# Performance work log

Hardware: AMD Instinct MI355X
Metric: run time of the kernel (lower is better)

## Reference

```python
import jax, jax.numpy as jnp
import numpy as np
import math

B, N, C = 4, 2048, 768
H = 12
DFF = 4 * C
EPS = 1e-5

def _layernorm(x, gamma, beta):
    mu = jnp.mean(x, axis=-1, keepdims=True)
    var = jnp.var(x, axis=-1, keepdims=True)
    return (x - mu) * jax.lax.rsqrt(var + EPS) * gamma + beta

def setup_inputs() -> dict:
    key = jax.random.key(0)
    ks = jax.random.split(key, 12)
    s = 0.02
    return {
        "x": jax.random.normal(ks[0], (B, N, C), jnp.float32),
        "Wqkv": jax.random.normal(ks[1], (C, 3 * C), jnp.float32) * s,
        "bqkv": jnp.zeros((3 * C,), jnp.float32),
        "Wproj": jax.random.normal(ks[2], (C, C), jnp.float32) * s,
        "bproj": jnp.zeros((C,), jnp.float32),
        "g1": jnp.ones((C,), jnp.float32),
        "b1": jnp.zeros((C,), jnp.float32),
        "g2": jnp.ones((C,), jnp.float32),
        "b2": jnp.zeros((C,), jnp.float32),
        "Wfc1": jax.random.normal(ks[3], (C, DFF), jnp.float32) * s,
        "bfc1": jnp.zeros((DFF,), jnp.float32),
        "Wfc2": jax.random.normal(ks[4], (DFF, C), jnp.float32) * s,
        "bfc2": jnp.zeros((C,), jnp.float32),
    }

def reference(x, Wqkv, bqkv, Wproj, bproj, g1, b1, g2, b2, Wfc1, bfc1, Wfc2, bfc2):
    head_dim = C // H
    qkv = x @ Wqkv + bqkv                      # [B,N,3C]
    q, k, v = jnp.split(qkv, 3, axis=-1)
    # [B,N,C] -> [B,H,N,hd]
    def to_heads(t):
        return t.reshape(B, N, H, head_dim).transpose(0, 2, 1, 3)
    q, k, v = to_heads(q), to_heads(k), to_heads(v)
    attn = jnp.einsum('bhqd,bhkd->bhqk', q, k) / math.sqrt(head_dim)
    attn = jax.nn.softmax(attn, axis=-1)       # dropout p=0 -> identity
    out = jnp.einsum('bhqk,bhkd->bhqd', attn, v)
    out = out.transpose(0, 2, 1, 3).reshape(B, N, C)
    out = out @ Wproj + bproj
    x = _layernorm(x + out, g1, b1)
    h = jax.nn.gelu(x @ Wfc1 + bfc1, approximate=False) @ Wfc2 + bfc2
    x = _layernorm(x + h, g2, b2)
    return x
```

## Files before the change

kernel.cpp:

```cpp
#include <hip/hip_runtime.h>

typedef __bf16 bf16;
typedef __bf16 bf16x2 __attribute__((ext_vector_type(2)));
typedef __bf16 bf16x4 __attribute__((ext_vector_type(4)));
typedef __bf16 bf16x8 __attribute__((ext_vector_type(8)));
typedef float  f32x4  __attribute__((ext_vector_type(4)));
typedef float  f32x16 __attribute__((ext_vector_type(16)));
typedef int    intx4  __attribute__((ext_vector_type(4)));

#define BB 4
#define SEQ 2048
#define CH 768
#define NH 12
#define HD 64
#define DFF 3072
#define MROWS (BB * SEQ)
#define C3 (3 * CH)

__device__ inline f32x16 mfma32(bf16x8 a, bf16x8 b, f32x16 c) {
    return __builtin_amdgcn_mfma_f32_32x32x16_bf16(a, b, c, 0, 0, 0);
}
__device__ inline f32x4 mfma16(bf16x8 a, bf16x8 b, f32x4 c) {
    return __builtin_amdgcn_mfma_f32_16x16x32_bf16(a, b, c, 0, 0, 0);
}
__device__ inline void gload16(const void* g, void* l) {
    __builtin_amdgcn_global_load_lds((const __attribute__((address_space(1))) void*)g,
                                     (__attribute__((address_space(3))) void*)l, 16, 0, 0);
}

__global__ void cvt_f32_bf16(const float* __restrict__ in, bf16* __restrict__ out, int n) {
    int i = (blockIdx.x * blockDim.x + threadIdx.x) * 4;
    if (i + 3 >= n) {
        for (int j = 0; j < 4 && i + j < n; ++j) out[i + j] = (bf16)in[i + j];
        return;
    }
    f32x4 v = *(const f32x4*)&in[i];
    bf16x4 o;
    #pragma unroll
    for (int j = 0; j < 4; ++j) o[j] = (bf16)v[j];
    *(bf16x4*)&out[i] = o;
}

__global__ void transpose_cvt(const float* __restrict__ in, bf16* __restrict__ out, int R, int Cc) {
    __shared__ bf16 t[32][33];
    int tx = threadIdx.x & 31, ty = threadIdx.x >> 5;
    int c0 = blockIdx.x * 32, r0 = blockIdx.y * 32;
    #pragma unroll
    for (int i = 0; i < 32; i += 8)
        t[ty + i][tx] = (bf16)in[(size_t)(r0 + ty + i) * Cc + c0 + tx];
    __syncthreads();
    #pragma unroll
    for (int i = 0; i < 32; i += 8)
        out[(size_t)(c0 + ty + i) * R + r0 + tx] = t[tx][ty + i];
}

__global__ void transpose_v(const bf16* __restrict__ qkvb, bf16* __restrict__ vt) {
    __shared__ bf16 t[32][33];
    int tx = threadIdx.x & 31, ty = threadIdx.x >> 5;
    int n0 = blockIdx.x * 32, d0 = blockIdx.y * 32, bh = blockIdx.z;
    int b = bh / NH, h = bh - b * NH;
    #pragma unroll
    for (int i = 0; i < 32; i += 8)
        t[ty + i][tx] = qkvb[((size_t)b * SEQ + n0 + ty + i) * C3 + 2 * CH + h * HD + d0 + tx];
    __syncthreads();
    #pragma unroll
    for (int i = 0; i < 32; i += 8)
        vt[((size_t)bh * HD + d0 + ty + i) * SEQ + n0 + tx] = t[tx][ty + i];
}

template <int OMODE>
__global__ __launch_bounds__(256) void gemm_bt(const bf16* __restrict__ A,
                                               const bf16* __restrict__ Bt,
                                               const float* __restrict__ bias,
                                               void* __restrict__ Cout,
                                               int M, int N, int K) {
    __shared__ __align__(16) bf16 As[128][32];
    __shared__ __align__(16) bf16 Bs[128][32];
    const int bm = blockIdx.y * 128, bn = blockIdx.x * 128;
    const int tid = threadIdx.x;
    const int lane = tid & 63, w = tid >> 6;
    const int wr = w >> 1, wc = w & 1;
    const int lr = lane & 15, lg = lane >> 4;

    const int srow = tid >> 2, schk = (tid & 3) * 8;
    const bf16* gA0 = A + (size_t)(bm + srow) * K + schk;
    const bf16* gA1 = A + (size_t)(bm + 64 + srow) * K + schk;
    const bf16* gB0 = Bt + (size_t)(bn + srow) * K + schk;
    const bf16* gB1 = Bt + (size_t)(bn + 64 + srow) * K + schk;
    bf16* lA0 = &As[srow][schk];
    bf16* lA1 = &As[64 + srow][schk];
    bf16* lB0 = &Bs[srow][schk];
    bf16* lB1 = &Bs[64 + srow][schk];

    f32x4 acc[4][4];
    #pragma unroll
    for (int i = 0; i < 4; ++i)
        #pragma unroll
        for (int j = 0; j < 4; ++j) acc[i][j] = (f32x4){0.f, 0.f, 0.f, 0.f};

    for (int k0 = 0; k0 < K; k0 += 32) {
        __syncthreads();
        gload16(gA0, lA0); gload16(gA1, lA1);
        gload16(gB0, lB0); gload16(gB1, lB1);
        gA0 += 32; gA1 += 32; gB0 += 32; gB1 += 32;
        __syncthreads();
        bf16x8 af[4], bfr[4];
        #pragma unroll
        for (int mi = 0; mi < 4; ++mi)
            af[mi] = *(const bf16x8*)&As[wr * 64 + mi * 16 + lr][lg * 8];
        #pragma unroll
        for (int ni = 0; ni < 4; ++ni)
            bfr[ni] = *(const bf16x8*)&Bs[wc * 64 + ni * 16 + lr][lg * 8];
        #pragma unroll
        for (int mi = 0; mi < 4; ++mi)
            #pragma unroll
            for (int ni = 0; ni < 4; ++ni)
                acc[mi][ni] = mfma16(af[mi], bfr[ni], acc[mi][ni]);
    }

    #pragma unroll
    for (int mi = 0; mi < 4; ++mi) {
        #pragma unroll
        for (int ni = 0; ni < 4; ++ni) {
            int col = bn + wc * 64 + ni * 16 + lr;
            float bsv = bias[col];
            #pragma unroll
            for (int r = 0; r < 4; ++r) {
                int row = bm + wr * 64 + mi * 16 + lg * 4 + r;
                float v = acc[mi][ni][r] + bsv;
                if (OMODE == 2) v = 0.5f * v * (1.0f + erff(v * 0.70710678118654752f));
                if (OMODE == 0)
                    ((float*)Cout)[(size_t)row * N + col] = v;
                else
                    ((bf16*)Cout)[(size_t)row * N + col] = (bf16)v;
            }
        }
    }
}

#define C2F 0.18033688011112f
#define THR2 11.5416f
__global__ __launch_bounds__(256, 3) void attn_kernel(const bf16* __restrict__ qkvb,
                                                      const bf16* __restrict__ vt,
                                                      bf16* __restrict__ outb) {
    __shared__ __align__(16) bf16 Kl[2][64 * 64];
    __shared__ __align__(16) bf16 Vl[2][64 * 64];
    const int tid = threadIdx.x;
    const int w = tid >> 6, lane = tid & 63;
    const int lq = lane & 31;
    const int hi = lane >> 5;
    const int lin = blockIdx.x;
    const int xcd = lin & 7, slot = lin >> 3;
    const int bh = xcd * 6 + (slot >> 4);
    const int qt = slot & 15;
    const int b = bh / NH, h = bh - b * NH;
    const int q0 = qt * 128 + w * 32;

    const bf16* qbase = qkvb + (size_t)b * SEQ * C3 + h * HD;
    const bf16* kbase = qbase + CH;
    const bf16* vbase = vt + (size_t)bh * HD * SEQ;

    const int srow = tid >> 3;
    const int ksc = (tid & 7) ^ (srow & 7);
    const bf16* gk0 = kbase + (size_t)srow * C3 + ksc * 8;
    const bf16* gk1 = kbase + (size_t)(srow + 32) * C3 + ksc * 8;
    const bf16* gv0 = vbase + (size_t)srow * SEQ + ksc * 8;
    const bf16* gv1 = vbase + (size_t)(srow + 32) * SEQ + ksc * 8;
    const int ldst = tid * 8;

    bf16x8 qf[4];
    #pragma unroll
    for (int ks = 0; ks < 4; ++ks)
        qf[ks] = *(const bf16x8*)&qbase[(size_t)(q0 + lq) * C3 + ks * 16 + hi * 8];

    f32x16 o0 = {0.f}, o1 = {0.f};
    float m = -3.0e38f, l = 0.f;

    const int swz = lq & 7;

    auto stage = [&](int buf, int kv0) {
        gload16(gk0 + (size_t)kv0 * C3, &Kl[buf][ldst]);
        gload16(gk1 + (size_t)kv0 * C3, &Kl[buf][2048 + ldst]);
        gload16(gv0 + kv0, &Vl[buf][ldst]);
        gload16(gv1 + kv0, &Vl[buf][2048 + ldst]);
    };

    auto process = [&](const bf16* Kb, const bf16* Vb) {
        f32x16 st0 = {0.f}, st1 = {0.f};
        #pragma unroll
        for (int ks = 0; ks < 4; ++ks) {
            int c = 8 * ((2 * ks + hi) ^ swz);
            bf16x8 k0 = *(const bf16x8*)&Kb[lq * 64 + c];
            bf16x8 k1 = *(const bf16x8*)&Kb[(32 + lq) * 64 + c];
            st0 = mfma32(k0, qf[ks], st0);
            st1 = mfma32(k1, qf[ks], st1);
        }
        float t_[8];
        #pragma unroll
        for (int r = 0; r < 8; ++r)
            t_[r] = fmaxf(fmaxf(st0[r], st0[r + 8]), fmaxf(st1[r], st1[r + 8]));
        #pragma unroll
        for (int r = 0; r < 4; ++r) t_[r] = fmaxf(t_[r], t_[r + 4]);
        float mx = fmaxf(fmaxf(t_[0], t_[1]), fmaxf(t_[2], t_[3]));
        mx = fmaxf(mx, __shfl_xor(mx, 32));
        float m2x = mx * C2F;
        if (!__all(m2x <= m + THR2)) {
            float mn = fmaxf(m, m2x);
            float alpha = __builtin_amdgcn_exp2f(m - mn);
            m = mn;
            l *= alpha;
            #pragma unroll
            for (int r = 0; r < 16; ++r) {
                int qr = (r & 3) + 8 * (r >> 2) + 4 * hi;
                float ar = __shfl(alpha, qr);
                o0[r] *= ar;
                o1[r] *= ar;
            }
        }
        bf16x8 pa[4];
        float ps0, ps1;
        {
            float p[16];
            #pragma unroll
            for (int r = 0; r < 16; ++r) p[r] = __builtin_amdgcn_exp2f(fmaf(st0[r], C2F, -m));
            float s0[8];
            #pragma unroll
            for (int r = 0; r < 8; ++r) s0[r] = p[r] + p[r + 8];
            #pragma unroll
            for (int r = 0; r < 4; ++r) s0[r] += s0[r + 4];
            ps0 = (s0[0] + s0[1]) + (s0[2] + s0[3]);
            int a[8];
            #pragma unroll
            for (int i = 0; i < 8; ++i) {
                bf16x2 t2 = {(bf16)p[2 * i], (bf16)p[2 * i + 1]};
                a[i] = __builtin_bit_cast(int, t2);
            }
            int d0 = __shfl_xor(hi ? a[0] : a[2], 32);
            int d1 = __shfl_xor(hi ? a[1] : a[3], 32);
            int d2 = __shfl_xor(hi ? a[4] : a[6], 32);
            int d3 = __shfl_xor(hi ? a[5] : a[7], 32);
            intx4 f0 = hi ? (intx4){d0, d1, a[2], a[3]} : (intx4){a[0], a[1], d0, d1};
            intx4 f1 = hi ? (intx4){d2, d3, a[6], a[7]} : (intx4){a[4], a[5], d2, d3};
            pa[0] = __builtin_bit_cast(bf16x8, f0);
            pa[1] = __builtin_bit_cast(bf16x8, f1);
        }
        {
            float p[16];
            #pragma unroll
            for (int r = 0; r < 16; ++r) p[r] = __builtin_amdgcn_exp2f(fmaf(st1[r], C2F, -m));
            float s0[8];
            #pragma unroll
            for (int r = 0; r < 8; ++r) s0[r] = p[r] + p[r + 8];
            #pragma unroll
            for (int r = 0; r < 4; ++r) s0[r] += s0[r + 4];
            ps1 = (s0[0] + s0[1]) + (s0[2] + s0[3]);
            int a[8];
            #pragma unroll
            for (int i = 0; i < 8; ++i) {
                bf16x2 t2 = {(bf16)p[2 * i], (bf16)p[2 * i + 1]};
                a[i] = __builtin_bit_cast(int, t2);
            }
            int d0 = __shfl_xor(hi ? a[0] : a[2], 32);
            int d1 = __shfl_xor(hi ? a[1] : a[3], 32);
            int d2 = __shfl_xor(hi ? a[4] : a[6], 32);
            int d3 = __shfl_xor(hi ? a[5] : a[7], 32);
            intx4 f0 = hi ? (intx4){d0, d1, a[2], a[3]} : (intx4){a[0], a[1], d0, d1};
            intx4 f1 = hi ? (intx4){d2, d3, a[6], a[7]} : (intx4){a[4], a[5], d2, d3};
            pa[2] = __builtin_bit_cast(bf16x8, f0);
            pa[3] = __builtin_bit_cast(bf16x8, f1);
        }
        float ps = ps0 + ps1;
        ps += __shfl_xor(ps, 32);
        l += ps;
        #pragma unroll
        for (int c = 0; c < 4; ++c) {
            int cc = 8 * ((2 * c + hi) ^ swz);
            bf16x8 v0 = *(const bf16x8*)&Vb[lq * 64 + cc];
            bf16x8 v1 = *(const bf16x8*)&Vb[(32 + lq) * 64 + cc];
            o0 = mfma32(pa[c], v0, o0);
            o1 = mfma32(pa[c], v1, o1);
        }
    };

    stage(0, 0);
    __syncthreads();
    for (int t = 0; t < 32; t += 2) {
        stage(1, (t + 1) * 64);
        process(Kl[0], Vl[0]);
        __syncthreads();
        stage(0, (t + 2 < 32 ? t + 2 : 31) * 64);
        process(Kl[1], Vl[1]);
        __syncthreads();
    }

    float linv = 1.0f / l;
    const size_t obase = (size_t)b * SEQ * CH + h * HD;
    #pragma unroll
    for (int r = 0; r < 16; ++r) {
        int qr = (r & 3) + 8 * (r >> 2) + 4 * hi;
        float lr_ = __shfl(linv, qr);
        size_t rowo = obase + (size_t)(q0 + qr) * CH;
        outb[rowo + lq] = (bf16)(o0[r] * lr_);
        outb[rowo + 32 + lq] = (bf16)(o1[r] * lr_);
    }
}

__global__ __launch_bounds__(256) void add_ln(const float* __restrict__ x,
                                              const float* __restrict__ t,
                                              const float* __restrict__ g,
                                              const float* __restrict__ bt,
                                              float* __restrict__ y,
                                              bf16* __restrict__ yb) {
    const int row = blockIdx.x;
    const size_t base = (size_t)row * CH;
    const int tid = threadIdx.x;
    float v[3];
    #pragma unroll
    for (int k = 0; k < 3; ++k) {
        int c = tid + k * 256;
        v[k] = x[base + c] + t[base + c];
    }
    __shared__ float red[4];
    float s = v[0] + v[1] + v[2];
    #pragma unroll
    for (int off = 32; off >= 1; off >>= 1) s += __shfl_down(s, off);
    if ((tid & 63) == 0) red[tid >> 6] = s;
    __syncthreads();
    float mean = (red[0] + red[1] + red[2] + red[3]) * (1.0f / 768.0f);
    float q = 0.f;
    #pragma unroll
    for (int k = 0; k < 3; ++k) {
        float d = v[k] - mean;
        q += d * d;
    }
    __syncthreads();
    #pragma unroll
    for (int off = 32; off >= 1; off >>= 1) q += __shfl_down(q, off);
    if ((tid & 63) == 0) red[tid >> 6] = q;
    __syncthreads();
    float var = (red[0] + red[1] + red[2] + red[3]) * (1.0f / 768.0f);
    float rstd = rsqrtf(var + 1e-5f);
    #pragma unroll
    for (int k = 0; k < 3; ++k) {
        int c = tid + k * 256;
        float out = (v[k] - mean) * rstd * g[c] + bt[c];
        y[base + c] = out;
        if (yb) yb[base + c] = (bf16)out;
    }
}

extern "C" void kernel_launch(void* const* d_in, const int* in_sizes, int n_in,
                              void* d_out, int out_size, void* d_ws, size_t ws_size,
                              hipStream_t stream) {
    const float* x    = (const float*)d_in[0];
    const float* Wqkv = (const float*)d_in[1];
    const float* bqkv = (const float*)d_in[2];
    const float* Wproj= (const float*)d_in[3];
    const float* bproj= (const float*)d_in[4];
    const float* g1   = (const float*)d_in[5];
    const float* b1   = (const float*)d_in[6];
    const float* g2   = (const float*)d_in[7];
    const float* b2   = (const float*)d_in[8];
    const float* Wfc1 = (const float*)d_in[9];
    const float* bfc1 = (const float*)d_in[10];
    const float* Wfc2 = (const float*)d_in[11];
    const float* bfc2 = (const float*)d_in[12];

    char* ws = (char*)d_ws;
    size_t off = 0;
    auto alloc = [&](size_t bytes) -> void* {
        void* p = ws + off;
        off += (bytes + 255) & ~(size_t)255;
        return p;
    };

    bf16* xb     = (bf16*)alloc((size_t)MROWS * CH * 2);
    bf16* WqkvT  = (bf16*)alloc((size_t)C3 * CH * 2);
    bf16* WprojT = (bf16*)alloc((size_t)CH * CH * 2);
    bf16* Wfc1T  = (bf16*)alloc((size_t)DFF * CH * 2);
    bf16* Wfc2T  = (bf16*)alloc((size_t)CH * DFF * 2);
    bf16* qkvb   = (bf16*)alloc((size_t)MROWS * C3 * 2);
    bf16* vtb    = (bf16*)alloc((size_t)BB * NH * HD * SEQ * 2);
    bf16* attnb  = (bf16*)alloc((size_t)MROWS * CH * 2);
    float* tmp   = (float*)alloc((size_t)MROWS * CH * 4);
    float* y1    = (float*)alloc((size_t)MROWS * CH * 4);
    bf16* y1b    = (bf16*)alloc((size_t)MROWS * CH * 2);
    bf16* hb     = (bf16*)alloc((size_t)MROWS * DFF * 2);

    cvt_f32_bf16<<<(MROWS * CH / 4 + 255) / 256, 256, 0, stream>>>(x, xb, MROWS * CH);
    transpose_cvt<<<dim3(C3 / 32, CH / 32), 256, 0, stream>>>(Wqkv, WqkvT, CH, C3);
    transpose_cvt<<<dim3(CH / 32, CH / 32), 256, 0, stream>>>(Wproj, WprojT, CH, CH);
    transpose_cvt<<<dim3(DFF / 32, CH / 32), 256, 0, stream>>>(Wfc1, Wfc1T, CH, DFF);
    transpose_cvt<<<dim3(CH / 32, DFF / 32), 256, 0, stream>>>(Wfc2, Wfc2T, DFF, CH);
    gemm_bt<1><<<dim3(C3 / 128, MROWS / 128), 256, 0, stream>>>(xb, WqkvT, bqkv, qkvb, MROWS, C3, CH);
    transpose_v<<<dim3(SEQ / 32, HD / 32, BB * NH), 256, 0, stream>>>(qkvb, vtb);
    attn_kernel<<<768, 256, 0, stream>>>(qkvb, vtb, attnb);
    gemm_bt<0><<<dim3(CH / 128, MROWS / 128), 256, 0, stream>>>(attnb, WprojT, bproj, tmp, MROWS, CH, CH);
    add_ln<<<MROWS, 256, 0, stream>>>(x, tmp, g1, b1, y1, y1b);
    gemm_bt<2><<<dim3(DFF / 128, MROWS / 128), 256, 0, stream>>>(y1b, Wfc1T, bfc1, hb, MROWS, DFF, CH);
    gemm_bt<0><<<dim3(CH / 128, MROWS / 128), 256, 0, stream>>>(hb, Wfc2T, bfc2, tmp, MROWS, CH, DFF);
    add_ln<<<MROWS, 256, 0, stream>>>(y1, tmp, g2, b2, (float*)d_out, nullptr);
}
```

Measured before the change: 353.4 us.

## Split-K the narrow projection GEMMs and remap workgroups for L2 locality

The two N=768 GEMMs (attention projection and FC2) now run as split-K with two K halves. Each half writes fp32 partials to its own buffer, and the following add+layernorm kernel sums the partials and adds the bias. The aim is to raise the workgroup count for these narrow GEMMs (only 384 tiles) so they fill the GPU better. All GEMMs also get a workgroup index remap that interleaves blocks across groups of 8, presumably to improve cache locality. The cost is extra fp32 partial-buffer writes and reads.

```diff
diff --git a/kernel.cpp b/kernel.cpp
--- a/kernel.cpp
+++ b/kernel.cpp
@@ -73,20 +73,24 @@
                                                const bf16* __restrict__ Bt,
                                                const float* __restrict__ bias,
                                                void* __restrict__ Cout,
-                                               int M, int N, int K) {
+                                               int M, int N, int K, int lda) {
     __shared__ __align__(16) bf16 As[128][32];
     __shared__ __align__(16) bf16 Bs[128][32];
-    const int bm = blockIdx.y * 128, bn = blockIdx.x * 128;
+    const int nwg = gridDim.x * gridDim.y;
+    const int orig = blockIdx.y * gridDim.x + blockIdx.x;
+    const int wg = (orig & 7) * (nwg >> 3) + (orig >> 3);
+    const int bm = (wg / gridDim.x) * 128, bn = (wg % gridDim.x) * 128;
+    const int kbeg = blockIdx.z * K;
     const int tid = threadIdx.x;
     const int lane = tid & 63, w = tid >> 6;
     const int wr = w >> 1, wc = w & 1;
     const int lr = lane & 15, lg = lane >> 4;
 
     const int srow = tid >> 2, schk = (tid & 3) * 8;
-    const bf16* gA0 = A + (size_t)(bm + srow) * K + schk;
-    const bf16* gA1 = A + (size_t)(bm + 64 + srow) * K + schk;
-    const bf16* gB0 = Bt + (size_t)(bn + srow) * K + schk;
-    const bf16* gB1 = Bt + (size_t)(bn + 64 + srow) * K + schk;
+    const bf16* gA0 = A + (size_t)(bm + srow) * lda + kbeg + schk;
+    const bf16* gA1 = A + (size_t)(bm + 64 + srow) * lda + kbeg + schk;
+    const bf16* gB0 = Bt + (size_t)(bn + srow) * lda + kbeg + schk;
+    const bf16* gB1 = Bt + (size_t)(bn + 64 + srow) * lda + kbeg + schk;
     bf16* lA0 = &As[srow][schk];
     bf16* lA1 = &As[64 + srow][schk];
     bf16* lB0 = &Bs[srow][schk];
@@ -118,19 +122,22 @@
                 acc[mi][ni] = mfma16(af[mi], bfr[ni], acc[mi][ni]);
     }
 
+    float* outp = (float*)Cout;
+    if (OMODE == 3) outp += (size_t)blockIdx.z * M * N;
+
     #pragma unroll
     for (int mi = 0; mi < 4; ++mi) {
         #pragma unroll
         for (int ni = 0; ni < 4; ++ni) {
             int col = bn + wc * 64 + ni * 16 + lr;
-            float bsv = bias[col];
+            float bsv = (OMODE == 3) ? 0.f : bias[col];
             #pragma unroll
             for (int r = 0; r < 4; ++r) {
                 int row = bm + wr * 64 + mi * 16 + lg * 4 + r;
                 float v = acc[mi][ni][r] + bsv;
                 if (OMODE == 2) v = 0.5f * v * (1.0f + erff(v * 0.70710678118654752f));
-                if (OMODE == 0)
-                    ((float*)Cout)[(size_t)row * N + col] = v;
+                if (OMODE == 0 || OMODE == 3)
+                    outp[(size_t)row * N + col] = v;
                 else
                     ((bf16*)Cout)[(size_t)row * N + col] = (bf16)v;
             }
@@ -306,7 +313,9 @@
 }
 
 __global__ __launch_bounds__(256) void add_ln(const float* __restrict__ x,
-                                              const float* __restrict__ t,
+                                              const float* __restrict__ t0,
+                                              const float* __restrict__ t1,
+                                              const float* __restrict__ bias,
                                               const float* __restrict__ g,
                                               const float* __restrict__ bt,
                                               float* __restrict__ y,
@@ -318,7 +327,10 @@
     #pragma unroll
     for (int k = 0; k < 3; ++k) {
         int c = tid + k * 256;
-        v[k] = x[base + c] + t[base + c];
+        float acc = x[base + c] + t0[base + c];
+        if (t1) acc += t1[base + c];
+        if (bias) acc += bias[c];
+        v[k] = acc;
     }
     __shared__ float red[4];
     float s = v[0] + v[1] + v[2];
@@ -382,7 +394,7 @@
     bf16* qkvb   = (bf16*)alloc((size_t)MROWS * C3 * 2);
     bf16* vtb    = (bf16*)alloc((size_t)BB * NH * HD * SEQ * 2);
     bf16* attnb  = (bf16*)alloc((size_t)MROWS * CH * 2);
-    float* tmp   = (float*)alloc((size_t)MROWS * CH * 4);
+    float* tmpP  = (float*)alloc((size_t)2 * MROWS * CH * 4);
     float* y1    = (float*)alloc((size_t)MROWS * CH * 4);
     bf16* y1b    = (bf16*)alloc((size_t)MROWS * CH * 2);
     bf16* hb     = (bf16*)alloc((size_t)MROWS * DFF * 2);
@@ -392,12 +404,12 @@
     transpose_cvt<<<dim3(CH / 32, CH / 32), 256, 0, stream>>>(Wproj, WprojT, CH, CH);
     transpose_cvt<<<dim3(DFF / 32, CH / 32), 256, 0, stream>>>(Wfc1, Wfc1T, CH, DFF);
     transpose_cvt<<<dim3(CH / 32, DFF / 32), 256, 0, stream>>>(Wfc2, Wfc2T, DFF, CH);
-    gemm_bt<1><<<dim3(C3 / 128, MROWS / 128), 256, 0, stream>>>(xb, WqkvT, bqkv, qkvb, MROWS, C3, CH);
+    gemm_bt<1><<<dim3(C3 / 128, MROWS / 128), 256, 0, stream>>>(xb, WqkvT, bqkv, qkvb, MROWS, C3, CH, CH);
     transpose_v<<<dim3(SEQ / 32, HD / 32, BB * NH), 256, 0, stream>>>(qkvb, vtb);
     attn_kernel<<<768, 256, 0, stream>>>(qkvb, vtb, attnb);
-    gemm_bt<0><<<dim3(CH / 128, MROWS / 128), 256, 0, stream>>>(attnb, WprojT, bproj, tmp, MROWS, CH, CH);
-    add_ln<<<MROWS, 256, 0, stream>>>(x, tmp, g1, b1, y1, y1b);
-    gemm_bt<2><<<dim3(DFF / 128, MROWS / 128), 256, 0, stream>>>(y1b, Wfc1T, bfc1, hb, MROWS, DFF, CH);
-    gemm_bt<0><<<dim3(CH / 128, MROWS / 128), 256, 0, stream>>>(hb, Wfc2T, bfc2, tmp, MROWS, CH, DFF);
-    add_ln<<<MROWS, 256, 0, stream>>>(y1, tmp, g2, b2, (float*)d_out, nullptr);
-}
+    gemm_bt<3><<<dim3(CH / 128, MROWS / 128, 2), 256, 0, stream>>>(attnb, WprojT, nullptr, tmpP, MROWS, CH, CH / 2, CH);
+    add_ln<<<MROWS, 256, 0, stream>>>(x, tmpP, tmpP + (size_t)MROWS * CH, bproj, g1, b1, y1, y1b);
+    gemm_bt<2><<<dim3(DFF / 128, MROWS / 128), 256, 0, stream>>>(y1b, Wfc1T, bfc1, hb, MROWS, DFF, CH, CH);
+    gemm_bt<3><<<dim3(CH / 128, MROWS / 128, 2), 256, 0, stream>>>(hb, Wfc2T, nullptr, tmpP, MROWS, CH, DFF / 2, DFF);
+    add_ln<<<MROWS, 256, 0, stream>>>(y1, tmpP, tmpP + (size_t)MROWS * CH, bfc2, g2, b2, (float*)d_out, nullptr);
+}
```

New measurement: 339.7 us. 3.9% less time.
